# Performance work log

Hardware: AMD Instinct MI355X
Metric: run time of the kernel (lower is better)

The kernel has to match this reference:

```python
import jax, jax.numpy as jnp
import numpy as np

OUT_H, OUT_W = 7, 7
SPATIAL_SCALE = 0.25
SAMPLING_RATIO = 2  # fixed sampling grid per bin (sampling_ratio > 0 branch)


def setup_inputs() -> dict:
    key = jax.random.key(0)
    k1, k2, k3, k4, k5 = jax.random.split(key, 5)
    B, C, H, W = 2, 256, 200, 200
    N = 1000
    features = jax.random.normal(k1, (B, C, H, W), dtype=jnp.float32)
    # rois: [batch_idx, cx, cy, w, h, theta] in IMAGE coords (image = 800x800 since scale=0.25)
    batch_idx = jax.random.randint(k2, (N,), 0, B).astype(jnp.float32)
    centers = jax.random.uniform(k3, (N, 2), minval=100.0, maxval=700.0)
    sizes = jax.random.uniform(k4, (N, 2), minval=32.0, maxval=256.0)
    angles = jax.random.uniform(k5, (N, 1), minval=0.0, maxval=float(np.pi))
    rois = jnp.concatenate([batch_idx[:, None], centers, sizes, angles], axis=1).astype(jnp.float32)
    return {"features": features, "rois": rois}


def _roi_align_rotated(features, rois, out_h, out_w, scale, g):
    B, C, H, W = features.shape
    N = rois.shape[0]
    b = rois[:, 0].astype(jnp.int32)
    cx = rois[:, 1] * scale
    cy = rois[:, 2] * scale
    rw = jnp.maximum(rois[:, 3] * scale, 1.0)
    rh = jnp.maximum(rois[:, 4] * scale, 1.0)
    theta = rois[:, 5]
    bin_h = rh / out_h
    bin_w = rw / out_w
    # sample offsets within the roi: yy = -h/2 + (s + 0.5) * bin/g for s in [0, out*g)
    sy = (jnp.arange(out_h * g, dtype=features.dtype) + 0.5) / g  # [Hs] in bin units
    sx = (jnp.arange(out_w * g, dtype=features.dtype) + 0.5) / g  # [Ws]
    yy = -rh[:, None] * 0.5 + sy[None, :] * bin_h[:, None]  # [N, Hs]
    xx = -rw[:, None] * 0.5 + sx[None, :] * bin_w[:, None]  # [N, Ws]
    cos_t = jnp.cos(theta)[:, None, None]
    sin_t = jnp.sin(theta)[:, None, None]
    # rotate around roi center (mmcv / detectron2 convention)
    y = yy[:, :, None] * cos_t - xx[:, None, :] * sin_t + cy[:, None, None]  # [N, Hs, Ws]
    x = yy[:, :, None] * sin_t + xx[:, None, :] * cos_t + cx[:, None, None]
    # bilinear_interpolate semantics from the CUDA kernel
    inside = (y >= -1.0) & (y <= H) & (x >= -1.0) & (x <= W)
    yc = jnp.clip(y, 0.0)
    xc = jnp.clip(x, 0.0)
    yl = jnp.minimum(jnp.floor(yc).astype(jnp.int32), H - 1)
    xl = jnp.minimum(jnp.floor(xc).astype(jnp.int32), W - 1)
    yh = jnp.minimum(yl + 1, H - 1)
    xh = jnp.minimum(xl + 1, W - 1)
    ly = jnp.where(jnp.floor(yc) >= H - 1, 0.0, yc - yl)
    lx = jnp.where(jnp.floor(xc) >= W - 1, 0.0, xc - xl)
    hy = 1.0 - ly
    hx = 1.0 - lx
    bi = b[:, None, None]
    v1 = features[bi, :, yl, xl]  # [N, Hs, Ws, C]
    v2 = features[bi, :, yl, xh]
    v3 = features[bi, :, yh, xl]
    v4 = features[bi, :, yh, xh]
    w1 = (hy * hx)[..., None]
    w2 = (hy * lx)[..., None]
    w3 = (ly * hx)[..., None]
    w4 = (ly * lx)[..., None]
    val = w1 * v1 + w2 * v2 + w3 * v3 + w4 * v4
    val = jnp.where(inside[..., None], val, 0.0)
    # average over the g x g samples per output bin
    val = val.reshape(N, out_h, g, out_w, g, C).mean(axis=(2, 4))  # [N, out_h, out_w, C]
    return jnp.transpose(val, (0, 3, 1, 2))  # [N, C, out_h, out_w]


def reference(features, rois):
    return _roi_align_rotated(features, rois, OUT_H, OUT_W, SPATIAL_SCALE, SAMPLING_RATIO)
```

## Files before the change

### kernel.cpp

```cpp
#include <hip/hip_runtime.h>
#include <hip/hip_fp16.h>


#define B_ 2
#define C_ 256
#define H_ 200
#define W_ 200
#define OUTHW 7
#define GRID_S 14
#define NSAMP 196
#define ELEMS (C_ * OUTHW * OUTHW)

__global__ __launch_bounds__(256) void transpose_h_kernel(
    const float* __restrict__ feat, __half* __restrict__ featT)
{
    __shared__ float tile[64][65];
    const int x0 = blockIdx.x * 64;
    const int c0 = blockIdx.y * 64;
    const int zz = blockIdx.z;
    const int b  = zz / 25;
    const int y0 = (zz - b * 25) * 8;
    const int t  = threadIdx.x;
    const int nx = min(64, W_ - x0);

    const int rr = t >> 4;
    const int jj = t & 15;
    const int ii = t >> 4;
    const int cq = (t & 15) * 4;

    for (int dy = 0; dy < 8; ++dy) {
        const int y = y0 + dy;
        if (jj * 4 < nx) {
            #pragma unroll
            for (int p = 0; p < 4; ++p) {
                const int cl = p * 16 + rr;
                const float4 v = *(const float4*)(feat +
                    ((size_t)(b * C_ + c0 + cl) * H_ + y) * W_ + x0 + jj * 4);
                *(float4*)&tile[cl][jj * 4] = v;
            }
        }
        __syncthreads();
        #pragma unroll
        for (int p = 0; p < 4; ++p) {
            const int i = p * 16 + ii;
            if (i < nx) {
                union { __half2 h2[2]; float2 f2; } u;
                u.h2[0] = __floats2half2_rn(tile[cq + 0][i], tile[cq + 1][i]);
                u.h2[1] = __floats2half2_rn(tile[cq + 2][i], tile[cq + 3][i]);
                *(float2*)(featT +
                    ((size_t)(b * H_ + y) * W_ + x0 + i) * C_ + c0 + cq) = u.f2;
            }
        }
        __syncthreads();
    }
}

__device__ __forceinline__ void build_table(
    const float* __restrict__ rois, int n, int t,
    float4* s_w4, int4* s_idx4, int byte_mode, int* s_b)
{
    const float spatial_scale = 0.25f;
    if (t == 0 && s_b) *s_b = (int)rois[n * 6 + 0];
    if (t < NSAMP) {
        const int   b  = (int)rois[n * 6 + 0];
        const float cx = rois[n * 6 + 1] * spatial_scale;
        const float cy = rois[n * 6 + 2] * spatial_scale;
        const float rw = fmaxf(rois[n * 6 + 3] * spatial_scale, 1.0f);
        const float rh = fmaxf(rois[n * 6 + 4] * spatial_scale, 1.0f);
        const float th = rois[n * 6 + 5];
        const float cosv = cosf(th), sinv = sinf(th);

        const float bin_h = rh * (1.0f / OUTHW);
        const float bin_w = rw * (1.0f / OUTHW);
        const int row = t / GRID_S;
        const int col = t % GRID_S;

        const float yy = -rh * 0.5f + ((float)row + 0.5f) * 0.5f * bin_h;
        const float xx = -rw * 0.5f + ((float)col + 0.5f) * 0.5f * bin_w;

        const float y = yy * cosv - xx * sinv + cy;
        const float x = yy * sinv + xx * cosv + cx;

        const bool inside = (y >= -1.0f) && (y <= (float)H_) &&
                            (x >= -1.0f) && (x <= (float)W_);

        const float yc = fmaxf(y, 0.0f);
        const float xc = fmaxf(x, 0.0f);
        const float fy = floorf(yc);
        const float fx = floorf(xc);
        int yl = min((int)fy, H_ - 1);
        int xl = min((int)fx, W_ - 1);
        const int yh = min(yl + 1, H_ - 1);
        const int xh = min(xl + 1, W_ - 1);
        const float ly = (fy >= (float)(H_ - 1)) ? 0.0f : (yc - fy);
        const float lx = (fx >= (float)(W_ - 1)) ? 0.0f : (xc - fx);
        const float hy = 1.0f - ly;
        const float hx = 1.0f - lx;

        const float m = inside ? 0.25f : 0.0f;
        s_w4[t] = make_float4(hy * hx * m, hy * lx * m, ly * hx * m, ly * lx * m);

        const int bb = byte_mode ? b : 0;
        const int scale = byte_mode ? (C_ * 2) : 1;
        s_idx4[t] = make_int4(((bb * H_ + yl) * W_ + xl) * scale,
                              ((bb * H_ + yl) * W_ + xh) * scale,
                              ((bb * H_ + yh) * W_ + xl) * scale,
                              ((bb * H_ + yh) * W_ + xh) * scale);
    }
}

template <int BC>
__device__ __forceinline__ void drain(
    const __half s_out[25][258], float* __restrict__ ob, int B0, int t)
{
    #pragma unroll
    for (int k = 0; k < BC; ++k) {
        const int m = t + k * 256;
        const int c = m / BC;
        const int j = m - c * BC;
        ob[c * 49 + B0 + j] =
            __half2float(s_out[j][(c & 3) * 64 + (c >> 2)]);
    }
}

__global__ __launch_bounds__(256) void roi_main_split(
    const __half* __restrict__ featT,
    const float* __restrict__ rois,
    float* __restrict__ out)
{
    __shared__ float4 s_w4[NSAMP];
    __shared__ int4   s_idx4[NSAMP];
    __shared__ __half s_out[25][258];

    const int n    = blockIdx.x >> 1;
    const int half = blockIdx.x & 1;
    const int B0   = half * 25;
    const int BC_r = half ? 24 : 25;
    const int t    = threadIdx.x;

    build_table(rois, n, t, s_w4, s_idx4, 1, nullptr);
    __syncthreads();

    const int lane = t & 63;
    const int wave = t >> 6;
    const char* __restrict__ fbase = (const char*)featT + lane * 8;

    for (int bin = B0 + wave; bin < B0 + BC_r; bin += 4) {
        const int oy = bin / OUTHW;
        const int ox = bin - oy * OUTHW;
        float a0 = 0.f, a1 = 0.f, a2 = 0.f, a3 = 0.f;
        #pragma unroll
        for (int j = 0; j < 2; ++j) {
            #pragma unroll
            for (int i = 0; i < 2; ++i) {
                const int s = (oy * 2 + j) * GRID_S + (ox * 2 + i);
                const float4 w = s_w4[s];
                const int4   ix = s_idx4[s];
                const float* wq = (const float*)&w;
                const int*   iq = (const int*)&ix;
                #pragma unroll
                for (int q = 0; q < 4; ++q) {
                    const float2 rv =
                        *(const float2*)(fbase + (unsigned)iq[q]);
                    const __half2* hp = (const __half2*)&rv;
                    const float2 fa = __half22float2(hp[0]);
                    const float2 fb = __half22float2(hp[1]);
                    a0 = fmaf(wq[q], fa.x, a0);
                    a1 = fmaf(wq[q], fa.y, a1);
                    a2 = fmaf(wq[q], fb.x, a2);
                    a3 = fmaf(wq[q], fb.y, a3);
                }
            }
        }
        const int jb = bin - B0;
        s_out[jb][0 * 64 + lane] = __float2half(a0);
        s_out[jb][1 * 64 + lane] = __float2half(a1);
        s_out[jb][2 * 64 + lane] = __float2half(a2);
        s_out[jb][3 * 64 + lane] = __float2half(a3);
    }
    __syncthreads();

    float* __restrict__ ob = out + (size_t)n * ELEMS;
    if (half == 0) drain<25>(s_out, ob, 0, t);
    else           drain<24>(s_out, ob, 25, t);
}

__global__ __launch_bounds__(256) void roi_main_nchw(
    const float* __restrict__ feat,
    const float* __restrict__ rois,
    float* __restrict__ out)
{
    const int n = blockIdx.x;
    const int t = threadIdx.x;
    __shared__ float4 s_w4[NSAMP];
    __shared__ int4   s_idx4[NSAMP];
    __shared__ int    s_b;

    build_table(rois, n, t, s_w4, s_idx4, 0, &s_b);
    __syncthreads();

    const float* __restrict__ fb = feat + (size_t)s_b * (size_t)(C_ * H_ * W_);
    float* __restrict__ ob = out + (size_t)n * (size_t)ELEMS;

    for (int e = t; e < ELEMS; e += 256) {
        const int c   = e / 49;
        const int bin = e - c * 49;
        const int oy  = bin / 7;
        const int ox  = bin - oy * 7;
        const float* __restrict__ fc = fb + c * (H_ * W_);
        float acc = 0.0f;
        #pragma unroll
        for (int j = 0; j < 2; ++j) {
            #pragma unroll
            for (int i = 0; i < 2; ++i) {
                const int s = (oy * 2 + j) * GRID_S + (ox * 2 + i);
                const float4 w = s_w4[s];
                const int4   ix = s_idx4[s];
                acc += w.x * fc[ix.x];
                acc += w.y * fc[ix.y];
                acc += w.z * fc[ix.z];
                acc += w.w * fc[ix.w];
            }
        }
        ob[e] = acc;
    }
}

extern "C" void kernel_launch(void* const* d_in, const int* in_sizes, int n_in,
                              void* d_out, int out_size, void* d_ws, size_t ws_size,
                              hipStream_t stream) {
    const float* feat = (const float*)d_in[0];
    const float* rois = (const float*)d_in[1];
    float* out = (float*)d_out;
    const int N = in_sizes[1] / 6;

    const size_t need = (size_t)B_ * H_ * W_ * C_ * sizeof(__half);
    if (ws_size >= need) {
        __half* featT = (__half*)d_ws;
        dim3 tg((W_ + 63) / 64, C_ / 64, B_ * 25);
        transpose_h_kernel<<<tg, 256, 0, stream>>>(feat, featT);
        roi_main_split<<<2 * N, 256, 0, stream>>>(featT, rois, out);
    } else {
        roi_main_nchw<<<N, 256, 0, stream>>>(feat, rois, out);
    }
}
```

Before: 196.7 us.

## Sort ROIs by batch and Morton tile, remap blocks across XCDs for locality

Adds a bitonic sort, fused into the transpose kernel as one extra block, that orders ROIs by batch index and a Morton code of their center tile. The main kernel then remaps block IDs so that each group of 8 consecutive blocks (likely one per XCD under round-robin dispatch) covers a contiguous run of sorted ROIs. The goal is to keep spatially nearby ROIs on the same XCD so they share L2 hits on the transposed fp16 feature map. The cost is an extra serial sort on one block and an indirection through the permutation array, and the fast path now only runs when N is at most 1024 and 2N is divisible by 8.

```diff
diff --git a/kernel.cpp b/kernel.cpp
--- a/kernel.cpp
+++ b/kernel.cpp
@@ -10,17 +10,61 @@
 #define GRID_S 14
 #define NSAMP 196
 #define ELEMS (C_ * OUTHW * OUTHW)
-
-__global__ __launch_bounds__(256) void transpose_h_kernel(
-    const float* __restrict__ feat, __half* __restrict__ featT)
-{
+#define FEATT_BYTES ((size_t)B_ * H_ * W_ * C_ * sizeof(__half))
+
+__global__ __launch_bounds__(256) void transpose_sort_kernel(
+    const float* __restrict__ feat, __half* __restrict__ featT,
+    const float* __restrict__ rois, int* __restrict__ perm, int nroi)
+{
+    const int t = threadIdx.x;
+
+    if (blockIdx.z == B_ * 25) {
+        if (blockIdx.x != 0 || blockIdx.y != 0) return;
+        __shared__ unsigned spack[1024];
+        for (int i = t; i < 1024; i += 256) {
+            unsigned pk = 0xFFFFFFFFu;
+            if (i < nroi) {
+                const int b  = (int)rois[i * 6 + 0];
+                const int cx = (int)(rois[i * 6 + 1] * 0.25f);
+                const int cy = (int)(rois[i * 6 + 2] * 0.25f);
+                const int tx = min(15, max(0, cx >> 4));
+                const int ty = min(15, max(0, cy >> 4));
+                unsigned m = 0;
+                #pragma unroll
+                for (int k = 0; k < 4; ++k)
+                    m |= (((unsigned)(ty >> k) & 1u) << (2 * k + 1)) |
+                         (((unsigned)(tx >> k) & 1u) << (2 * k));
+                pk = ((((unsigned)b << 8) | m) << 10) | (unsigned)i;
+            }
+            spack[i] = pk;
+        }
+        __syncthreads();
+        for (unsigned k = 2; k <= 1024; k <<= 1) {
+            for (unsigned j = k >> 1; j > 0; j >>= 1) {
+                for (unsigned i = t; i < 1024; i += 256) {
+                    const unsigned ixj = i ^ j;
+                    if (ixj > i) {
+                        const unsigned a = spack[i], c = spack[ixj];
+                        const bool asc = ((i & k) == 0);
+                        if (asc ? (a > c) : (a < c)) {
+                            spack[i] = c; spack[ixj] = a;
+                        }
+                    }
+                }
+                __syncthreads();
+            }
+        }
+        for (int i = t; i < nroi; i += 256)
+            perm[i] = (int)(spack[i] & 1023u);
+        return;
+    }
+
     __shared__ float tile[64][65];
     const int x0 = blockIdx.x * 64;
     const int c0 = blockIdx.y * 64;
     const int zz = blockIdx.z;
     const int b  = zz / 25;
     const int y0 = (zz - b * 25) * 8;
-    const int t  = threadIdx.x;
     const int nx = min(64, W_ - x0);
 
     const int rr = t >> 4;
@@ -126,14 +170,17 @@
 __global__ __launch_bounds__(256) void roi_main_split(
     const __half* __restrict__ featT,
     const float* __restrict__ rois,
-    float* __restrict__ out)
+    const int* __restrict__ perm,
+    float* __restrict__ out,
+    int slots)
 {
     __shared__ float4 s_w4[NSAMP];
     __shared__ int4   s_idx4[NSAMP];
     __shared__ __half s_out[25][258];
 
-    const int n    = blockIdx.x >> 1;
-    const int half = blockIdx.x & 1;
+    const int h    = (blockIdx.x & 7) * slots + (blockIdx.x >> 3);
+    const int n    = perm[h >> 1];
+    const int half = h & 1;
     const int B0   = half * 25;
     const int BC_r = half ? 24 : 25;
     const int t    = threadIdx.x;
@@ -234,12 +281,15 @@
     float* out = (float*)d_out;
     const int N = in_sizes[1] / 6;
 
-    const size_t need = (size_t)B_ * H_ * W_ * C_ * sizeof(__half);
-    if (ws_size >= need) {
+    const bool can = (ws_size >= FEATT_BYTES + 4096) &&
+                     (N >= 1) && (N <= 1024) && ((2 * N) % 8 == 0);
+    if (can) {
         __half* featT = (__half*)d_ws;
-        dim3 tg((W_ + 63) / 64, C_ / 64, B_ * 25);
-        transpose_h_kernel<<<tg, 256, 0, stream>>>(feat, featT);
-        roi_main_split<<<2 * N, 256, 0, stream>>>(featT, rois, out);
+        int* perm = (int*)((char*)d_ws + FEATT_BYTES);
+        dim3 tg((W_ + 63) / 64, C_ / 64, B_ * 25 + 1);
+        transpose_sort_kernel<<<tg, 256, 0, stream>>>(feat, featT, rois, perm, N);
+        roi_main_split<<<2 * N, 256, 0, stream>>>(featT, rois, perm, out,
+                                                  (2 * N) / 8);
     } else {
         roi_main_nchw<<<N, 256, 0, stream>>>(feat, rois, out);
     }
```

New measurement: 188.8 us. 4.0% less time.
